# Kernel tuning notes

Measured on AMD Instinct MI355X. Metric: run time of the kernel, lower is better.

The kernel has to match this reference:

```python
import jax, jax.numpy as jnp
import numpy as np

B, S, D, H = 2, 2048, 1024, 16
HD = D // H  # 64

def _make_freqs():
    # flux-style rotation matrices: [1,1,S,HD//2,2,2]
    theta = 10000.0
    inv = 1.0 / (theta ** (np.arange(0, HD, 2, dtype=np.float32) / HD))  # [HD//2]
    pos = np.arange(S, dtype=np.float32)
    ang = pos[:, None] * inv[None, :]  # [S, HD//2]
    cos, sin = np.cos(ang), np.sin(ang)
    rot = np.stack([np.stack([cos, -sin], -1), np.stack([sin, cos], -1)], -2)  # [S,HD//2,2,2]
    return jnp.asarray(rot[None, None], dtype=jnp.float32)

def setup_inputs() -> dict:
    key = jax.random.key(0)
    ks = jax.random.split(key, 9)
    sc = 1.0 / np.sqrt(D)
    return {
        "x": jax.random.normal(ks[0], (B, S, D), jnp.float32),
        "freqs": _make_freqs(),
        "Wq": jax.random.normal(ks[1], (D, D), jnp.float32) * sc,
        "bq": jax.random.normal(ks[2], (D,), jnp.float32) * 0.01,
        "Wk": jax.random.normal(ks[3], (D, D), jnp.float32) * sc,
        "bk": jax.random.normal(ks[4], (D,), jnp.float32) * 0.01,
        "Wv": jax.random.normal(ks[5], (D, D), jnp.float32) * sc,
        "bv": jax.random.normal(ks[6], (D,), jnp.float32) * 0.01,
        "Wo": jax.random.normal(ks[7], (D, D), jnp.float32) * sc,
        "bo": jax.random.normal(ks[8], (D,), jnp.float32) * 0.01,
    }

def _apply_rope(xq, xk, freqs):
    # xq/xk: [B,H,S,HD]; freqs: [1,1,S,HD//2,2,2]
    def rot(t):
        t_ = t.reshape(*t.shape[:-1], -1, 1, 2)  # [B,H,S,HD//2,1,2]
        out = freqs[..., 0] * t_[..., 0] + freqs[..., 1] * t_[..., 1]  # [B,H,S,HD//2,2]
        return out.reshape(t.shape).astype(t.dtype)
    return rot(xq), rot(xk)

def reference(x, freqs, Wq, bq, Wk, bk, Wv, bv, Wo, bo):
    b, s, _ = x.shape
    # QKV projections (torch Linear: x @ W.T + b)
    q = (x @ Wq.T + bq).reshape(b, s, H, HD).transpose(0, 2, 1, 3)  # [B,H,S,HD]
    k = (x @ Wk.T + bk).reshape(b, s, H, HD).transpose(0, 2, 1, 3)
    v = (x @ Wv.T + bv).reshape(b, s, H, HD).transpose(0, 2, 1, 3)
    q, k = _apply_rope(q, k, freqs)
    # scaled dot product attention, no mask, no dropout
    scale = 1.0 / jnp.sqrt(jnp.asarray(HD, x.dtype))
    scores = jnp.einsum("bhqd,bhkd->bhqk", q, k) * scale
    attn = jax.nn.softmax(scores, axis=-1)
    o = jnp.einsum("bhqk,bhkd->bhqd", attn, v)  # [B,H,S,HD]
    o = o.transpose(0, 2, 1, 3).reshape(b, s, D)
    return o @ Wo.T + bo
```

## Files before the change

kernel.cpp:

```cpp
#include <hip/hip_runtime.h>
#include <cmath>

#define B_ 2
#define S_ 2048
#define D_ 1024
#define H_ 16
#define HD_ 64
#define M_ 4096

typedef __attribute__((ext_vector_type(8))) short short8;
typedef __attribute__((ext_vector_type(4))) short short4v;
typedef __attribute__((ext_vector_type(4))) float f32x4;

__device__ __forceinline__ short f2bf(float x) {
    unsigned u = __builtin_bit_cast(unsigned, x);
    u += 0x7fffu + ((u >> 16) & 1u);
    return (short)(u >> 16);
}

__device__ __forceinline__ void gload_lds16(const short* g, short* l) {
    __builtin_amdgcn_global_load_lds(
        (const __attribute__((address_space(1))) unsigned int*)g,
        (__attribute__((address_space(3))) unsigned int*)l, 16, 0, 0);
}

template<int N> __device__ __forceinline__ void vwait() {
    if constexpr (N == 0) asm volatile("s_waitcnt vmcnt(0)" ::: "memory");
    else if constexpr (N == 2) asm volatile("s_waitcnt vmcnt(2)" ::: "memory");
    else if constexpr (N == 3) asm volatile("s_waitcnt vmcnt(3)" ::: "memory");
    else if constexpr (N == 4) asm volatile("s_waitcnt vmcnt(4)" ::: "memory");
}
__device__ __forceinline__ void bar() { __builtin_amdgcn_s_barrier(); }

__global__ __launch_bounds__(256) void cast_all_kernel(
    const float* __restrict__ x,  const float* __restrict__ Wq,
    const float* __restrict__ Wk, const float* __restrict__ Wv,
    const float* __restrict__ Wo,
    short* __restrict__ xb, short* __restrict__ Wqkvb, short* __restrict__ Wob)
{
    const size_t i = (size_t)blockIdx.x * 256 + threadIdx.x;
    const float* src; short* dst; size_t off;
    if (i < 1048576)      { src = x;  dst = xb;              off = i; }
    else if (i < 1310720) { src = Wq; dst = Wqkvb;           off = i - 1048576; }
    else if (i < 1572864) { src = Wk; dst = Wqkvb + 1048576; off = i - 1310720; }
    else if (i < 1835008) { src = Wv; dst = Wqkvb + 2097152; off = i - 1572864; }
    else                  { src = Wo; dst = Wob;             off = i - 1835008; }
    float4 v = ((const float4*)src)[off];
    short4v o = { f2bf(v.x), f2bf(v.y), f2bf(v.z), f2bf(v.w) };
    ((short4v*)dst)[off] = o;
}

template<int MODE, int TM, int TN>
__global__ __launch_bounds__(256) void gemm_sa2(
    const short* __restrict__ A, const short* __restrict__ Bw,
    const float* __restrict__ b0p, const float* __restrict__ b1p, const float* __restrict__ b2p,
    const float* __restrict__ freqs,
    void* __restrict__ out0, void* __restrict__ out1, void* __restrict__ out2)
{
    constexpr int RT = TM / 32, CT = TN / 32;
    constexpr int LPC = TM/64 + TN/64;
    __shared__ __align__(16) short A0[TM*32];
    __shared__ __align__(16) short A1[TM*32];
    __shared__ __align__(16) short A2[TM*32];
    __shared__ __align__(16) short B0[TN*32];
    __shared__ __align__(16) short B1[TN*32];
    __shared__ __align__(16) short B2[TN*32];
    const int t = threadIdx.x;
    const int w = t >> 6;
    const int lane = t & 63;
    const int qd = lane >> 4, l = lane & 15;
    const int n0 = blockIdx.x * TN, m0 = blockIdx.y * TM;
    const int wr = (w >> 1) * (TM/2), wc = (w & 1) * (TN/2);
    const int srow  = lane >> 2;
    const int sslot = ((lane & 3) ^ ((lane >> 3) & 3)) * 8;
    const int rsw = (l >> 1) & 3;

    f32x4 acc[RT][CT] = {};

    auto STAGE = [&](int c, short* As, short* Bss) {
        const int k0 = c * 32;
        #pragma unroll
        for (int j = 0; j < TM/64; ++j) {
            const int r0 = (j*4 + w) * 16;
            gload_lds16(A + (size_t)(m0 + r0 + srow)*1024 + k0 + sslot, &As[r0*32]);
        }
        #pragma unroll
        for (int j = 0; j < TN/64; ++j) {
            const int r0 = (j*4 + w) * 16;
            gload_lds16(Bw + (size_t)(n0 + r0 + srow)*1024 + k0 + sslot, &Bss[r0*32]);
        }
    };

    auto COMP = [&](const short* As, const short* Bss) {
        short8 af[RT], bfr[CT];
        #pragma unroll
        for (int rt = 0; rt < RT; ++rt)
            af[rt] = *(const short8*)&As[(wr + rt*16 + l)*32 + ((qd ^ rsw) << 3)];
        #pragma unroll
        for (int ct = 0; ct < CT; ++ct)
            bfr[ct] = *(const short8*)&Bss[(wc + ct*16 + l)*32 + ((qd ^ rsw) << 3)];
        #pragma unroll
        for (int rt = 0; rt < RT; ++rt)
            #pragma unroll
            for (int ct = 0; ct < CT; ++ct)
                acc[rt][ct] = __builtin_amdgcn_mfma_f32_16x16x32_bf16(af[rt], bfr[ct], acc[rt][ct], 0, 0, 0);
    };

    STAGE(0, A0, B0);
    STAGE(1, A1, B1);
    for (int p = 0; p <= 27; p += 3) {
        vwait<LPC>(); bar();
        STAGE(p + 2, A2, B2);
        COMP(A0, B0);
        vwait<LPC>(); bar();
        STAGE(p + 3, A0, B0);
        COMP(A1, B1);
        vwait<LPC>(); bar();
        STAGE(p + 4, A1, B1);
        COMP(A2, B2);
    }
    vwait<LPC>(); bar();
    COMP(A0, B0);
    vwait<0>(); bar();
    COMP(A1, B1);

    if (MODE == 0) {
        float* out = (float*)out0;
        #pragma unroll
        for (int rt = 0; rt < RT; ++rt)
            #pragma unroll
            for (int ct = 0; ct < CT; ++ct) {
                const int n = n0 + wc + ct*16 + l;
                const float bias = b0p[n];
                #pragma unroll
                for (int r = 0; r < 4; ++r) {
                    const int m = m0 + wr + rt*16 + qd*4 + r;
                    out[(size_t)m*1024 + n] = acc[rt][ct][r] + bias;
                }
            }
    } else {
        const int sel = n0 >> 10;
        const int nb = n0 & 1023;
        const float* bias = (sel == 0) ? b0p : (sel == 1) ? b1p : b2p;
        if (sel < 2) {
            short* outg = (short*)((sel == 0) ? out0 : out1);
            #pragma unroll
            for (int rt = 0; rt < RT; ++rt)
                #pragma unroll
                for (int ct = 0; ct < CT; ++ct) {
                    const int d = nb + wc + ct*16 + l;
                    const float bsv = bias[d];
                    const int h = d >> 6, hd = d & 63;
                    #pragma unroll
                    for (int r = 0; r < 4; ++r) {
                        const int m = m0 + wr + rt*16 + qd*4 + r;
                        const int bb = m >> 11, s = m & 2047;
                        float val = acc[rt][ct][r] + bsv;
                        float pv = __shfl_xor(val, 1);
                        const float* f = freqs + (size_t)s*128 + (size_t)(hd >> 1)*4;
                        float o = (d & 1) ? (f[2]*pv + f[3]*val) : (f[0]*val + f[1]*pv);
                        outg[((size_t)(bb*16 + h)*2048 + s)*64 + hd] = f2bf(o);
                    }
                }
        } else {
            short* outv = (short*)out2;
            #pragma unroll
            for (int rt = 0; rt < RT; ++rt)
                #pragma unroll
                for (int ct = 0; ct < CT; ++ct) {
                    const int d = nb + wc + ct*16 + l;
                    const float bsv = bias[d];
                    const int h = d >> 6, hd = d & 63;
                    const int m0r = m0 + wr + rt*16 + qd*4;
                    const int bb = m0r >> 11, s0 = m0r & 2047;
                    short4v pk;
                    #pragma unroll
                    for (int r = 0; r < 4; ++r) pk[r] = f2bf(acc[rt][ct][r] + bsv);
                    *(short4v*)&outv[((size_t)(bb*16 + h)*64 + hd)*2048 + s0] = pk;
                }
        }
    }
}

__global__ __launch_bounds__(512) void attn_mfma(
    const short* __restrict__ qg, const short* __restrict__ kg,
    const short* __restrict__ vtg, short* __restrict__ og)
{
    __shared__ __align__(16) short K0[64*64];
    __shared__ __align__(16) short K1[64*64];
    __shared__ __align__(16) short K2[64*64];
    __shared__ __align__(16) short V0[64*64];
    __shared__ __align__(16) short V1[64*64];
    __shared__ __align__(16) short V2[64*64];
    __shared__ __align__(16) short Pb[128*64];

    const int t = threadIdx.x;
    const int w = t >> 6;
    const int lane = t & 63;
    const int qd = lane >> 4, l = lane & 15;
    const int l7 = lane & 7;
    const int q0 = blockIdx.x * 128;
    const int bh = blockIdx.y;

    const int rl  = lane >> 3;
    const int ss8 = ((lane & 7) ^ rl) << 3;

    short8 qf[2];
    const short* qb = qg + ((size_t)bh*2048 + q0 + w*16)*64;
    #pragma unroll
    for (int kf = 0; kf < 2; ++kf)
        qf[kf] = *(const short8*)&qb[l*64 + kf*32 + qd*8];

    f32x4 oacc[4] = {};
    float lsum = 0.f;

    const short* kbase = kg  + (size_t)bh*2048*64;
    const short* vbase = vtg + (size_t)bh*64*2048;
    const float SC = 0.125f * 1.44269504088896340736f;

    auto PREF = [&](int c, short* Kd, short* Vd) {
        gload_lds16(kbase + (size_t)(c*64 + w*8 + rl)*64 + ss8,   &Kd[(w*8)*64]);
        gload_lds16(vbase + (size_t)(w*8 + rl)*2048 + c*64 + ss8, &Vd[(w*8)*64]);
    };

    auto TILE = [&](const short* Kc, const short* Vc) {
        f32x4 sacc[4] = {};
        #pragma unroll
        for (int ct = 0; ct < 4; ++ct) {
            short8 k0f = *(const short8*)&Kc[(ct*16 + l)*64 + (((0 + qd) ^ l7) << 3)];
            short8 k1f = *(const short8*)&Kc[(ct*16 + l)*64 + (((4 + qd) ^ l7) << 3)];
            sacc[ct] = __builtin_amdgcn_mfma_f32_16x16x32_bf16(k0f, qf[0], sacc[ct], 0, 0, 0);
            sacc[ct] = __builtin_amdgcn_mfma_f32_16x16x32_bf16(k1f, qf[1], sacc[ct], 0, 0, 0);
        }
        #pragma unroll
        for (int ct = 0; ct < 4; ++ct) {
            float p0 = exp2f(sacc[ct][0] * SC);
            float p1 = exp2f(sacc[ct][1] * SC);
            float p2 = exp2f(sacc[ct][2] * SC);
            float p3 = exp2f(sacc[ct][3] * SC);
            lsum += (p0 + p1) + (p2 + p3);
            union { unsigned u[2]; short4v s; } cv;
            asm("v_cvt_pk_bf16_f32 %0, %1, %2" : "=v"(cv.u[0]) : "v"(p0), "v"(p1));
            asm("v_cvt_pk_bf16_f32 %0, %1, %2" : "=v"(cv.u[1]) : "v"(p2), "v"(p3));
            *(short4v*)&Pb[(w*16 + l)*64 + (((ct*32 + qd*8) ^ (l7 << 4)) >> 1)] = cv.s;
        }
        #pragma unroll
        for (int kf = 0; kf < 2; ++kf) {
            const int so = ((kf*4 + qd) ^ l7) << 3;
            short8 pa = *(const short8*)&Pb[(w*16 + l)*64 + so];
            #pragma unroll
            for (int ht = 0; ht < 4; ++ht) {
                short8 vb = *(const short8*)&Vc[(ht*16 + l)*64 + so];
                oacc[ht] = __builtin_amdgcn_mfma_f32_16x16x32_bf16(pa, vb, oacc[ht], 0, 0, 0);
            }
        }
    };

    PREF(0, K0, V0);
    PREF(1, K1, V1);
    for (int p = 0; p <= 27; p += 3) {
        vwait<2>(); bar();
        PREF(p + 2, K2, V2);
        TILE(K0, V0);
        vwait<2>(); bar();
        PREF(p + 3, K0, V0);
        TILE(K1, V1);
        vwait<2>(); bar();
        PREF(p + 4, K1, V1);
        TILE(K2, V2);
    }
    vwait<2>(); bar();
    TILE(K0, V0);
    vwait<0>(); bar();
    TILE(K1, V1);

    lsum += __shfl_xor(lsum, 16);
    lsum += __shfl_xor(lsum, 32);
    float inv[4];
    #pragma unroll
    for (int r = 0; r < 4; ++r)
        inv[r] = 1.0f / __shfl(lsum, qd*4 + r);

    const int bb = bh >> 4, h = bh & 15;
    #pragma unroll
    for (int ht = 0; ht < 4; ++ht)
        #pragma unroll
        for (int r = 0; r < 4; ++r) {
            const int s = q0 + w*16 + qd*4 + r;
            og[((size_t)bb*2048 + s)*1024 + h*64 + ht*16 + l] =
                f2bf(oacc[ht][r] * inv[r]);
        }
}

extern "C" void kernel_launch(void* const* d_in, const int* in_sizes, int n_in,
                              void* d_out, int out_size, void* d_ws, size_t ws_size,
                              hipStream_t stream)
{
    const float* x  = (const float*)d_in[0];
    const float* fr = (const float*)d_in[1];
    const float* Wq = (const float*)d_in[2];
    const float* bq = (const float*)d_in[3];
    const float* Wk = (const float*)d_in[4];
    const float* bk = (const float*)d_in[5];
    const float* Wv = (const float*)d_in[6];
    const float* bv = (const float*)d_in[7];
    const float* Wo = (const float*)d_in[8];
    const float* bo = (const float*)d_in[9];
    float* out = (float*)d_out;

    short* ws    = (short*)d_ws;
    short* xb    = ws;
    short* Wqkvb = xb    + 4194304;
    short* Wob   = Wqkvb + 3145728;
    short* qg    = Wob   + 1048576;
    short* kg    = qg    + 4194304;
    short* vtg   = kg    + 4194304;
    short* og    = vtg   + 4194304;

    cast_all_kernel<<<8192, 256, 0, stream>>>(x, Wq, Wk, Wv, Wo, xb, Wqkvb, Wob);
    gemm_sa2<1,128,128><<<dim3(24, 32), 256, 0, stream>>>(xb, Wqkvb, bq, bk, bv, fr, qg, kg, vtg);
    attn_mfma<<<dim3(16, 32), 512, 0, stream>>>(qg, kg, vtg, og);
    gemm_sa2<0,128,64><<<dim3(16, 32), 256, 0, stream>>>(og, Wob, bo, nullptr, nullptr, nullptr,
                                                         out, nullptr, nullptr);
}
```

Before: 239.1 us.

## Use 256x256-tile 512-thread GEMM with XCD-aware block mapping for QKV projection

```diff
diff --git a/kernel.cpp b/kernel.cpp
--- a/kernel.cpp
+++ b/kernel.cpp
@@ -50,12 +50,122 @@
     ((short4v*)dst)[off] = o;
 }
 
-template<int MODE, int TM, int TN>
-__global__ __launch_bounds__(256) void gemm_sa2(
+__global__ __launch_bounds__(512) void gemm256(
     const short* __restrict__ A, const short* __restrict__ Bw,
     const float* __restrict__ b0p, const float* __restrict__ b1p, const float* __restrict__ b2p,
     const float* __restrict__ freqs,
-    void* __restrict__ out0, void* __restrict__ out1, void* __restrict__ out2)
+    short* __restrict__ out0, short* __restrict__ out1, short* __restrict__ out2)
+{
+    __shared__ __align__(16) short A0[256*32];
+    __shared__ __align__(16) short A1[256*32];
+    __shared__ __align__(16) short A2[256*32];
+    __shared__ __align__(16) short B0[256*32];
+    __shared__ __align__(16) short B1[256*32];
+    __shared__ __align__(16) short B2[256*32];
+    const int t = threadIdx.x;
+    const int w = t >> 6;
+    const int lane = t & 63;
+    const int qd = lane >> 4, l = lane & 15;
+    const int bid = blockIdx.x;
+    const int wg  = (bid & 7) * 24 + (bid >> 3);
+    const int n0 = (wg % 12) * 256;
+    const int m0 = (wg / 12) * 256;
+    const int wr = (w >> 2) * 128;
+    const int wc = (w & 3) * 64;
+    const int srow  = lane >> 2;
+    const int sslot = ((lane & 3) ^ ((lane >> 3) & 3)) * 8;
+    const int rsw = (l >> 1) & 3;
+
+    f32x4 acc[8][4] = {};
+
+    auto STAGE = [&](int c, short* As, short* Bss) {
+        const int k0 = c * 32;
+        #pragma unroll
+        for (int j = 0; j < 2; ++j) {
+            const int r0 = (j*8 + w) * 16;
+            gload_lds16(A  + (size_t)(m0 + r0 + srow)*1024 + k0 + sslot, &As[r0*32]);
+            gload_lds16(Bw + (size_t)(n0 + r0 + srow)*1024 + k0 + sslot, &Bss[r0*32]);
+        }
+    };
+
+    auto COMP = [&](const short* As, const short* Bss) {
+        short8 af[8], bfr[4];
+        #pragma unroll
+        for (int rt = 0; rt < 8; ++rt)
+            af[rt] = *(const short8*)&As[(wr + rt*16 + l)*32 + ((qd ^ rsw) << 3)];
+        #pragma unroll
+        for (int ct = 0; ct < 4; ++ct)
+            bfr[ct] = *(const short8*)&Bss[(wc + ct*16 + l)*32 + ((qd ^ rsw) << 3)];
+        #pragma unroll
+        for (int rt = 0; rt < 8; ++rt)
+            #pragma unroll
+            for (int ct = 0; ct < 4; ++ct)
+                acc[rt][ct] = __builtin_amdgcn_mfma_f32_16x16x32_bf16(af[rt], bfr[ct], acc[rt][ct], 0, 0, 0);
+    };
+
+    STAGE(0, A0, B0);
+    STAGE(1, A1, B1);
+    for (int p = 0; p <= 27; p += 3) {
+        vwait<4>(); bar();
+        STAGE(p + 2, A2, B2);
+        COMP(A0, B0);
+        vwait<4>(); bar();
+        STAGE(p + 3, A0, B0);
+        COMP(A1, B1);
+        vwait<4>(); bar();
+        STAGE(p + 4, A1, B1);
+        COMP(A2, B2);
+    }
+    vwait<4>(); bar();
+    COMP(A0, B0);
+    vwait<0>(); bar();
+    COMP(A1, B1);
+
+    const int sel = n0 >> 10;
+    const int nb = n0 & 1023;
+    const float* bias = (sel == 0) ? b0p : (sel == 1) ? b1p : b2p;
+    if (sel < 2) {
+        short* outg = (sel == 0) ? out0 : out1;
+        #pragma unroll
+        for (int rt = 0; rt < 8; ++rt)
+            #pragma unroll
+            for (int ct = 0; ct < 4; ++ct) {
+                const int d = nb + wc + ct*16 + l;
+                const float bsv = bias[d];
+                const int h = d >> 6, hd = d & 63;
+                #pragma unroll
+                for (int r = 0; r < 4; ++r) {
+                    const int m = m0 + wr + rt*16 + qd*4 + r;
+                    const int bb = m >> 11, s = m & 2047;
+                    float val = acc[rt][ct][r] + bsv;
+                    float pv = __shfl_xor(val, 1);
+                    const float* f = freqs + (size_t)s*128 + (size_t)(hd >> 1)*4;
+                    float o = (d & 1) ? (f[2]*pv + f[3]*val) : (f[0]*val + f[1]*pv);
+                    outg[((size_t)(bb*16 + h)*2048 + s)*64 + hd] = f2bf(o);
+                }
+            }
+    } else {
+        #pragma unroll
+        for (int rt = 0; rt < 8; ++rt)
+            #pragma unroll
+            for (int ct = 0; ct < 4; ++ct) {
+                const int d = nb + wc + ct*16 + l;
+                const float bsv = bias[d];
+                const int h = d >> 6, hd = d & 63;
+                const int m0r = m0 + wr + rt*16 + qd*4;
+                const int bb = m0r >> 11, s0 = m0r & 2047;
+                short4v pk;
+                #pragma unroll
+                for (int r = 0; r < 4; ++r) pk[r] = f2bf(acc[rt][ct][r] + bsv);
+                *(short4v*)&out2[((size_t)(bb*16 + h)*64 + hd)*2048 + s0] = pk;
+            }
+    }
+}
+
+template<int TM, int TN>
+__global__ __launch_bounds__(256) void gemm_sa2(
+    const short* __restrict__ A, const short* __restrict__ Bw,
+    const float* __restrict__ b0p, float* __restrict__ out)
 {
     constexpr int RT = TM / 32, CT = TN / 32;
     constexpr int LPC = TM/64 + TN/64;
@@ -124,62 +234,18 @@
     vwait<0>(); bar();
     COMP(A1, B1);
 
-    if (MODE == 0) {
-        float* out = (float*)out0;
-        #pragma unroll
-        for (int rt = 0; rt < RT; ++rt)
-            #pragma unroll
-            for (int ct = 0; ct < CT; ++ct) {
-                const int n = n0 + wc + ct*16 + l;
-                const float bias = b0p[n];
-                #pragma unroll
-                for (int r = 0; r < 4; ++r) {
-                    const int m = m0 + wr + rt*16 + qd*4 + r;
-                    out[(size_t)m*1024 + n] = acc[rt][ct][r] + bias;
-                }
+    #pragma unroll
+    for (int rt = 0; rt < RT; ++rt)
+        #pragma unroll
+        for (int ct = 0; ct < CT; ++ct) {
+            const int n = n0 + wc + ct*16 + l;
+            const float bias = b0p[n];
+            #pragma unroll
+            for (int r = 0; r < 4; ++r) {
+                const int m = m0 + wr + rt*16 + qd*4 + r;
+                out[(size_t)m*1024 + n] = acc[rt][ct][r] + bias;
             }
-    } else {
-        const int sel = n0 >> 10;
-        const int nb = n0 & 1023;
-        const float* bias = (sel == 0) ? b0p : (sel == 1) ? b1p : b2p;
-        if (sel < 2) {
-            short* outg = (short*)((sel == 0) ? out0 : out1);
-            #pragma unroll
-            for (int rt = 0; rt < RT; ++rt)
-                #pragma unroll
-                for (int ct = 0; ct < CT; ++ct) {
-                    const int d = nb + wc + ct*16 + l;
-                    const float bsv = bias[d];
-                    const int h = d >> 6, hd = d & 63;
-                    #pragma unroll
-                    for (int r = 0; r < 4; ++r) {
-                        const int m = m0 + wr + rt*16 + qd*4 + r;
-                        const int bb = m >> 11, s = m & 2047;
-                        float val = acc[rt][ct][r] + bsv;
-                        float pv = __shfl_xor(val, 1);
-                        const float* f = freqs + (size_t)s*128 + (size_t)(hd >> 1)*4;
-                        float o = (d & 1) ? (f[2]*pv + f[3]*val) : (f[0]*val + f[1]*pv);
-                        outg[((size_t)(bb*16 + h)*2048 + s)*64 + hd] = f2bf(o);
-                    }
-                }
-        } else {
-            short* outv = (short*)out2;
-            #pragma unroll
-            for (int rt = 0; rt < RT; ++rt)
-                #pragma unroll
-                for (int ct = 0; ct < CT; ++ct) {
-                    const int d = nb + wc + ct*16 + l;
-                    const float bsv = bias[d];
-                    const int h = d >> 6, hd = d & 63;
-                    const int m0r = m0 + wr + rt*16 + qd*4;
-                    const int bb = m0r >> 11, s0 = m0r & 2047;
-                    short4v pk;
-                    #pragma unroll
-                    for (int r = 0; r < 4; ++r) pk[r] = f2bf(acc[rt][ct][r] + bsv);
-                    *(short4v*)&outv[((size_t)(bb*16 + h)*64 + hd)*2048 + s0] = pk;
-                }
-        }
-    }
+        }
 }
 
 __global__ __launch_bounds__(512) void attn_mfma(
@@ -318,8 +384,7 @@
     short* og    = vtg   + 4194304;
 
     cast_all_kernel<<<8192, 256, 0, stream>>>(x, Wq, Wk, Wv, Wo, xb, Wqkvb, Wob);
-    gemm_sa2<1,128,128><<<dim3(24, 32), 256, 0, stream>>>(xb, Wqkvb, bq, bk, bv, fr, qg, kg, vtg);
+    gemm256<<<192, 512, 0, stream>>>(xb, Wqkvb, bq, bk, bv, fr, qg, kg, vtg);
     attn_mfma<<<dim3(16, 32), 512, 0, stream>>>(qg, kg, vtg, og);
-    gemm_sa2<0,128,64><<<dim3(16, 32), 256, 0, stream>>>(og, Wob, bo, nullptr, nullptr, nullptr,
-                                                         out, nullptr, nullptr);
-}
+    gemm_sa2<128,64><<<dim3(16, 32), 256, 0, stream>>>(og, Wob, bo, out);
+}
```

New measurement: 246.8 us. 3.2% more time.
